# Kernel tuning notes

Hardware: AMD Instinct MI355X
Metric: run time of the kernel (lower is better)

The kernel has to match this reference:

```python
import jax, jax.numpy as jnp
import numpy as np

N_DRUGS = 4096
W_DIM = 512
N_SUB = 10
N_EDGES = 131072


def setup_inputs() -> dict:
    key = jax.random.key(0)
    k1, k2, k3, k4 = jax.random.split(key, 4)
    z_drug = jax.random.normal(k1, (N_DRUGS, W_DIM), dtype=jnp.float32)
    # glorot-ish init for weights
    global_weight = jax.random.normal(k2, (W_DIM, W_DIM), dtype=jnp.float32) * (2.0 / (2 * W_DIM)) ** 0.5
    local_diag = jax.random.normal(k3, (N_SUB, W_DIM), dtype=jnp.float32) * (2.0 / (W_DIM + 1)) ** 0.5
    batch_edges = jax.random.randint(k4, (2, N_EDGES), 0, N_DRUGS, dtype=jnp.int64)
    return {
        "z_drug": z_drug,
        "global_weight": global_weight,
        "local_diag": local_diag,
        "batch_edges": batch_edges,
        "edge_sub_type_idx": 2,
    }


def reference(z_drug, global_weight, local_diag, batch_edges, edge_sub_type_idx):
    # edge_type == 'drug_drug': z1 = z2 = z_drug
    row_embed = z_drug[batch_edges[0]]            # [B, D]
    col_embed = z_drug[batch_edges[1]]            # [B, D]
    d = local_diag[edge_sub_type_idx]             # [D] diagonal of local weight matrix
    # row @ diag(d) @ W @ diag(d) == ((row * d) @ W) * d
    p = ((row_embed * d) @ global_weight) * d     # [B, D]
    # diagonal(p @ col^T) == rowwise dot product
    score = jnp.sum(p * col_embed, axis=-1)       # [B]
    return jax.nn.sigmoid(score)
```

## Files before the change

kernel.cpp:

```cpp
#include <hip/hip_runtime.h>
#include <cstdint>

#define ND 4096
#define D  512

typedef __bf16 bf16x8 __attribute__((ext_vector_type(8)));
typedef float floatx4 __attribute__((ext_vector_type(4)));
typedef unsigned short ushort8 __attribute__((ext_vector_type(8)));

__device__ __forceinline__ float bf2f(unsigned short b) {
    return __uint_as_float(((unsigned int)b) << 16);
}
__device__ __forceinline__ unsigned short f2bf(float f) {
    unsigned int u = __float_as_uint(f);
    u += 0x7fffu + ((u >> 16) & 1u);
    return (unsigned short)(u >> 16);
}
__device__ __forceinline__ float lo16(unsigned int u) { return __uint_as_float(u << 16); }
__device__ __forceinline__ float hi16(unsigned int u) { return __uint_as_float(u & 0xffff0000u); }

__device__ __forceinline__ void gll16(const void* g, void* l) {
    __builtin_amdgcn_global_load_lds((const __attribute__((address_space(1))) unsigned int*)g,
                                     (__attribute__((address_space(3))) unsigned int*)l,
                                     16, 0, 0);
}

union U8B8 { ushort8 u; bf16x8 b; };

__global__ __launch_bounds__(256) void detect_kernel(const unsigned short* __restrict__ z,
                                                     const int* __restrict__ ed,
                                                     int* __restrict__ flags) {
    __shared__ int c0, c1;
    if (threadIdx.x == 0) { c0 = 0; c1 = 0; }
    __syncthreads();
    unsigned short u = z[threadIdx.x];
    int e = (u >> 7) & 0xFF;
    if (e >= 96 && e <= 160) atomicAdd(&c0, 1);
    if (threadIdx.x < 64 && ed[2 * threadIdx.x + 1] == 0) atomicAdd(&c1, 1);
    __syncthreads();
    if (threadIdx.x == 0) {
        flags[0] = (c0 >= 240) ? 1 : 0;
        flags[1] = (c1 >= 56) ? 1 : 0;
    }
}

__global__ __launch_bounds__(256) void make_mt(const void* __restrict__ Wv,
                                               const void* __restrict__ ldv,
                                               const int* __restrict__ sub,
                                               unsigned short* __restrict__ Mt,
                                               const int* __restrict__ flags) {
    __shared__ float lds[64][65];
    int bf = flags[0];
    int su = sub[0];
    if ((unsigned)su > 9u) su = 2;
    int k0 = blockIdx.x * 64, n0 = blockIdx.y * 64;
    int j = threadIdx.x & 63;
    int w = threadIdx.x >> 6;

#pragma unroll
    for (int r = 0; r < 16; r++) {
        int k = k0 + w * 16 + r;
        float v = bf ? bf2f(((const unsigned short*)Wv)[k * D + n0 + j])
                     : ((const float*)Wv)[k * D + n0 + j];
        lds[w * 16 + r][j] = v;
    }
    __syncthreads();

    int k = k0 + j;
    float dk = bf ? bf2f(((const unsigned short*)ldv)[su * D + k])
                  : ((const float*)ldv)[su * D + k];
#pragma unroll
    for (int r = 0; r < 16; r++) {
        int n = n0 + w * 16 + r;
        float dn = bf ? bf2f(((const unsigned short*)ldv)[su * D + n])
                      : ((const float*)ldv)[su * D + n];
        Mt[n * D + k] = f2bf(lds[j][w * 16 + r] * dk * dn);
    }
}

template <bool BF>
__device__ void gemm_body(const void* __restrict__ z,
                          const unsigned short* __restrict__ Mt,
                          unsigned short* __restrict__ Y) {
    __shared__ __bf16 As[64 * 64];
    __shared__ __bf16 Bs[64 * 64];
    int tid = threadIdx.x;
    int w = tid >> 6, lane = tid & 63;
    int rl = lane & 15, quad = lane >> 4;
    int tm = blockIdx.x * 64, tn = blockIdx.y * 64;
    int wm = (w >> 1) * 32, wn = (w & 1) * 32;

    floatx4 acc[2][2] = {};
    for (int kk = 0; kk < D; kk += 64) {
        __syncthreads();
#pragma unroll
        for (int jj = 0; jj < 2; jj++) {
            int rowB = tn + w * 16 + jj * 8 + (lane >> 3);
            int col  = kk + (lane & 7) * 8;
            gll16(Mt + rowB * D + col, &Bs[(w * 16 + jj * 8) * 64]);
            if constexpr (BF) {
                int rowA = tm + w * 16 + jj * 8 + (lane >> 3);
                gll16((const __bf16*)z + rowA * D + col, &As[(w * 16 + jj * 8) * 64]);
            } else {
                int rowA = tm + w * 16 + jj * 8 + (lane >> 3);
                const float* zf = (const float*)z + rowA * D + col;
                float4 f0 = *(const float4*)zf;
                float4 f1 = *(const float4*)(zf + 4);
                U8B8 cv;
                cv.u[0] = f2bf(f0.x); cv.u[1] = f2bf(f0.y); cv.u[2] = f2bf(f0.z); cv.u[3] = f2bf(f0.w);
                cv.u[4] = f2bf(f1.x); cv.u[5] = f2bf(f1.y); cv.u[6] = f2bf(f1.z); cv.u[7] = f2bf(f1.w);
                *(bf16x8*)&As[(w * 16 + jj * 8 + (lane >> 3)) * 64 + (lane & 7) * 8] = cv.b;
            }
        }
        __syncthreads();
#pragma unroll
        for (int kc = 0; kc < 64; kc += 32) {
            bf16x8 a0 = *(const bf16x8*)&As[(wm + rl) * 64 + kc + quad * 8];
            bf16x8 a1 = *(const bf16x8*)&As[(wm + 16 + rl) * 64 + kc + quad * 8];
            bf16x8 b0 = *(const bf16x8*)&Bs[(wn + rl) * 64 + kc + quad * 8];
            bf16x8 b1 = *(const bf16x8*)&Bs[(wn + 16 + rl) * 64 + kc + quad * 8];
            acc[0][0] = __builtin_amdgcn_mfma_f32_16x16x32_bf16(a0, b0, acc[0][0], 0, 0, 0);
            acc[0][1] = __builtin_amdgcn_mfma_f32_16x16x32_bf16(a0, b1, acc[0][1], 0, 0, 0);
            acc[1][0] = __builtin_amdgcn_mfma_f32_16x16x32_bf16(a1, b0, acc[1][0], 0, 0, 0);
            acc[1][1] = __builtin_amdgcn_mfma_f32_16x16x32_bf16(a1, b1, acc[1][1], 0, 0, 0);
        }
    }
#pragma unroll
    for (int j = 0; j < 2; j++) {
        int col = tn + wn + j * 16 + rl;
#pragma unroll
        for (int i = 0; i < 2; i++) {
            int rbase = tm + wm + i * 16 + quad * 4;
#pragma unroll
            for (int r = 0; r < 4; r++)
                Y[(rbase + r) * D + col] = f2bf(acc[i][j][r]);
        }
    }
}

__global__ __launch_bounds__(256) void gemm_kernel(const void* __restrict__ z,
                                                   const unsigned short* __restrict__ Mt,
                                                   unsigned short* __restrict__ Y,
                                                   const int* __restrict__ flags) {
    if (flags[0]) gemm_body<true>(z, Mt, Y);
    else          gemm_body<false>(z, Mt, Y);
}

__global__ __launch_bounds__(256) void edge_pass(const unsigned short* __restrict__ Y,
                                                 const void* __restrict__ z,
                                                 const int* __restrict__ ed,
                                                 float* __restrict__ partial,
                                                 void* __restrict__ out,
                                                 int E,
                                                 const int* __restrict__ flags,
                                                 int pass) {
    int wid = (blockIdx.x * 256 + threadIdx.x) >> 6;
    int lane = threadIdx.x & 63;
    int h = lane >> 5, l = lane & 31;
    int e = wid * 2 + h;
    if (e >= E) return;
    int bf = flags[0];
    int r, c;
    if (flags[1]) { r = ed[2 * e]; c = ed[2 * (E + e)]; }
    else          { r = ed[e];     c = ed[E + e]; }
    r &= ND - 1; c &= ND - 1;

    int col = pass * 256 + l * 8;
    uint4 yu = *(const uint4*)(Y + r * D + col);
    float y0 = lo16(yu.x), y1 = hi16(yu.x), y2 = lo16(yu.y), y3 = hi16(yu.y);
    float y4 = lo16(yu.z), y5 = hi16(yu.z), y6 = lo16(yu.w), y7 = hi16(yu.w);
    float s;
    if (bf) {
        uint4 zu = *(const uint4*)((const unsigned short*)z + c * D + col);
        s  = y0 * lo16(zu.x) + y1 * hi16(zu.x);
        s += y2 * lo16(zu.y) + y3 * hi16(zu.y);
        s += y4 * lo16(zu.z) + y5 * hi16(zu.z);
        s += y6 * lo16(zu.w) + y7 * hi16(zu.w);
    } else {
        const float* zf = (const float*)z + c * D + col;
        float4 f0 = *(const float4*)zf;
        float4 f1 = *(const float4*)(zf + 4);
        s  = y0 * f0.x + y1 * f0.y + y2 * f0.z + y3 * f0.w;
        s += y4 * f1.x + y5 * f1.y + y6 * f1.z + y7 * f1.w;
    }
#pragma unroll
    for (int off = 16; off; off >>= 1)
        s += __shfl_xor(s, off, 64);

    if (l == 0) {
        if (pass == 0) {
            partial[e] = s;
        } else {
            float t = s + partial[e];
            if (!(t > -1e30f && t < 1e30f)) t = 0.0f;
            float sig = 1.0f / (1.0f + __expf(-t));
            if (bf) ((unsigned short*)out)[e] = f2bf(sig);
            else    ((float*)out)[e] = sig;
        }
    }
}

extern "C" void kernel_launch(void* const* d_in, const int* in_sizes, int n_in,
                              void* d_out, int out_size, void* d_ws, size_t ws_size,
                              hipStream_t stream) {
    const void* z     = d_in[0];
    const void* W     = d_in[1];
    const void* ldiag = d_in[2];
    const int* edges  = (const int*)d_in[3];
    const int* sub    = (const int*)d_in[4];
    int E = out_size;

    char* ws = (char*)d_ws;
    unsigned short* Y  = (unsigned short*)ws;
    unsigned short* Mt = (unsigned short*)(ws + 4194304);
    int* flags         = (int*)(ws + 4194304 + 524288);
    float* partial     = (float*)(ws + 4194304 + 524288 + 256);

    detect_kernel<<<1, 256, 0, stream>>>((const unsigned short*)z, edges, flags);
    make_mt<<<dim3(D / 64, D / 64), 256, 0, stream>>>(W, ldiag, sub, Mt, flags);
    gemm_kernel<<<dim3(ND / 64, D / 64), 256, 0, stream>>>(z, Mt, Y, flags);
    int eblocks = (E / 2 + 3) / 4;
    edge_pass<<<eblocks, 256, 0, stream>>>(Y, z, edges, partial, d_out, E, flags, 0);
    edge_pass<<<eblocks, 256, 0, stream>>>(Y, z, edges, partial, d_out, E, flags, 1);
}
```

Before: 122.1 us.

## Inline dtype detection per kernel, re-layout GEMM LDS, split edge pass into four

Drops the separate detection kernel: each kernel now derives the bf16 and int64 flags itself with a wave ballot over the first 64 elements, which removes one launch and the flag round-trip. The GEMM shared-memory tiles switch to a k-block-major layout so each global_load_lds writes 64 rows of one 8-element chunk, changing the LDS read pattern. The edge pass is templated on dtype and index width, uses 16 lanes per edge, and runs in four column slices with partial sums accumulated in memory, so each pass touches a smaller slice of Y and z. This trades one fewer launch for two extra edge launches and extra partial read-modify-write traffic.

Measured after the change: 126.7 us. 3.7% more time.

```diff
diff --git a/kernel.cpp b/kernel.cpp
--- a/kernel.cpp
+++ b/kernel.cpp
@@ -27,30 +27,27 @@
 
 union U8B8 { ushort8 u; bf16x8 b; };
 
-__global__ __launch_bounds__(256) void detect_kernel(const unsigned short* __restrict__ z,
-                                                     const int* __restrict__ ed,
-                                                     int* __restrict__ flags) {
-    __shared__ int c0, c1;
-    if (threadIdx.x == 0) { c0 = 0; c1 = 0; }
-    __syncthreads();
-    unsigned short u = z[threadIdx.x];
+__device__ __forceinline__ int2 detect_flags(const unsigned short* z, const int* ed) {
+    int lane = threadIdx.x & 63;
+    unsigned short u = z[lane];
     int e = (u >> 7) & 0xFF;
-    if (e >= 96 && e <= 160) atomicAdd(&c0, 1);
-    if (threadIdx.x < 64 && ed[2 * threadIdx.x + 1] == 0) atomicAdd(&c1, 1);
-    __syncthreads();
-    if (threadIdx.x == 0) {
-        flags[0] = (c0 >= 240) ? 1 : 0;
-        flags[1] = (c1 >= 56) ? 1 : 0;
-    }
+    unsigned long long b0 = __ballot(e >= 96 && e <= 160);
+    unsigned long long b1 = __ballot(ed[2 * lane + 1] == 0);
+    int2 f;
+    f.x = (__popcll(b0) >= 56) ? 1 : 0;
+    f.y = (__popcll(b1) >= 56) ? 1 : 0;
+    return f;
 }
 
 __global__ __launch_bounds__(256) void make_mt(const void* __restrict__ Wv,
                                                const void* __restrict__ ldv,
                                                const int* __restrict__ sub,
                                                unsigned short* __restrict__ Mt,
-                                               const int* __restrict__ flags) {
+                                               const unsigned short* __restrict__ zdet,
+                                               const int* __restrict__ eddet) {
     __shared__ float lds[64][65];
-    int bf = flags[0];
+    int2 f = detect_flags(zdet, eddet);
+    int bf = f.x;
     int su = sub[0];
     if ((unsigned)su > 9u) su = 2;
     int k0 = blockIdx.x * 64, n0 = blockIdx.y * 64;
@@ -82,8 +79,8 @@
 __device__ void gemm_body(const void* __restrict__ z,
                           const unsigned short* __restrict__ Mt,
                           unsigned short* __restrict__ Y) {
-    __shared__ __bf16 As[64 * 64];
-    __shared__ __bf16 Bs[64 * 64];
+    __shared__ __bf16 As[8 * 512];
+    __shared__ __bf16 Bs[8 * 512];
     int tid = threadIdx.x;
     int w = tid >> 6, lane = tid & 63;
     int rl = lane & 15, quad = lane >> 4;
@@ -94,31 +91,29 @@
     for (int kk = 0; kk < D; kk += 64) {
         __syncthreads();
 #pragma unroll
-        for (int jj = 0; jj < 2; jj++) {
-            int rowB = tn + w * 16 + jj * 8 + (lane >> 3);
-            int col  = kk + (lane & 7) * 8;
-            gll16(Mt + rowB * D + col, &Bs[(w * 16 + jj * 8) * 64]);
+        for (int t = 0; t < 2; t++) {
+            int kb = w * 2 + t;
+            gll16(Mt + (tn + lane) * D + kk + kb * 8, Bs + kb * 512);
             if constexpr (BF) {
-                int rowA = tm + w * 16 + jj * 8 + (lane >> 3);
-                gll16((const __bf16*)z + rowA * D + col, &As[(w * 16 + jj * 8) * 64]);
+                gll16((const __bf16*)z + (tm + lane) * D + kk + kb * 8, As + kb * 512);
             } else {
-                int rowA = tm + w * 16 + jj * 8 + (lane >> 3);
-                const float* zf = (const float*)z + rowA * D + col;
+                const float* zf = (const float*)z + (tm + lane) * D + kk + kb * 8;
                 float4 f0 = *(const float4*)zf;
                 float4 f1 = *(const float4*)(zf + 4);
                 U8B8 cv;
                 cv.u[0] = f2bf(f0.x); cv.u[1] = f2bf(f0.y); cv.u[2] = f2bf(f0.z); cv.u[3] = f2bf(f0.w);
                 cv.u[4] = f2bf(f1.x); cv.u[5] = f2bf(f1.y); cv.u[6] = f2bf(f1.z); cv.u[7] = f2bf(f1.w);
-                *(bf16x8*)&As[(w * 16 + jj * 8 + (lane >> 3)) * 64 + (lane & 7) * 8] = cv.b;
+                *(bf16x8*)(As + kb * 512 + lane * 8) = cv.b;
             }
         }
         __syncthreads();
 #pragma unroll
         for (int kc = 0; kc < 64; kc += 32) {
-            bf16x8 a0 = *(const bf16x8*)&As[(wm + rl) * 64 + kc + quad * 8];
-            bf16x8 a1 = *(const bf16x8*)&As[(wm + 16 + rl) * 64 + kc + quad * 8];
-            bf16x8 b0 = *(const bf16x8*)&Bs[(wn + rl) * 64 + kc + quad * 8];
-            bf16x8 b1 = *(const bf16x8*)&Bs[(wn + 16 + rl) * 64 + kc + quad * 8];
+            int kb0 = kc >> 3;
+            bf16x8 a0 = *(const bf16x8*)(As + (kb0 + quad) * 512 + (wm + rl) * 8);
+            bf16x8 a1 = *(const bf16x8*)(As + (kb0 + quad) * 512 + (wm + 16 + rl) * 8);
+            bf16x8 b0 = *(const bf16x8*)(Bs + (kb0 + quad) * 512 + (wn + rl) * 8);
+            bf16x8 b1 = *(const bf16x8*)(Bs + (kb0 + quad) * 512 + (wn + 16 + rl) * 8);
             acc[0][0] = __builtin_amdgcn_mfma_f32_16x16x32_bf16(a0, b0, acc[0][0], 0, 0, 0);
             acc[0][1] = __builtin_amdgcn_mfma_f32_16x16x32_bf16(a0, b1, acc[0][1], 0, 0, 0);
             acc[1][0] = __builtin_amdgcn_mfma_f32_16x16x32_bf16(a1, b0, acc[1][0], 0, 0, 0);
@@ -141,36 +136,35 @@
 __global__ __launch_bounds__(256) void gemm_kernel(const void* __restrict__ z,
                                                    const unsigned short* __restrict__ Mt,
                                                    unsigned short* __restrict__ Y,
-                                                   const int* __restrict__ flags) {
-    if (flags[0]) gemm_body<true>(z, Mt, Y);
-    else          gemm_body<false>(z, Mt, Y);
-}
-
-__global__ __launch_bounds__(256) void edge_pass(const unsigned short* __restrict__ Y,
-                                                 const void* __restrict__ z,
-                                                 const int* __restrict__ ed,
-                                                 float* __restrict__ partial,
-                                                 void* __restrict__ out,
-                                                 int E,
-                                                 const int* __restrict__ flags,
-                                                 int pass) {
-    int wid = (blockIdx.x * 256 + threadIdx.x) >> 6;
+                                                   const int* __restrict__ eddet) {
+    int2 f = detect_flags((const unsigned short*)z, eddet);
+    if (f.x) gemm_body<true>(z, Mt, Y);
+    else     gemm_body<false>(z, Mt, Y);
+}
+
+template <bool BF, bool I64>
+__device__ void edge_body(const unsigned short* __restrict__ Y,
+                          const void* __restrict__ z,
+                          const int* __restrict__ ed,
+                          float* __restrict__ partial,
+                          void* __restrict__ out,
+                          int E, int pass) {
+    int gid = blockIdx.x * 256 + threadIdx.x;
     int lane = threadIdx.x & 63;
-    int h = lane >> 5, l = lane & 31;
-    int e = wid * 2 + h;
+    int e = (gid >> 6) * 4 + (lane >> 4);
+    int l = lane & 15;
     if (e >= E) return;
-    int bf = flags[0];
     int r, c;
-    if (flags[1]) { r = ed[2 * e]; c = ed[2 * (E + e)]; }
-    else          { r = ed[e];     c = ed[E + e]; }
+    if constexpr (I64) { r = ed[2 * e]; c = ed[2 * (E + e)]; }
+    else               { r = ed[e];     c = ed[E + e]; }
     r &= ND - 1; c &= ND - 1;
 
-    int col = pass * 256 + l * 8;
+    int col = pass * 128 + l * 8;
     uint4 yu = *(const uint4*)(Y + r * D + col);
     float y0 = lo16(yu.x), y1 = hi16(yu.x), y2 = lo16(yu.y), y3 = hi16(yu.y);
     float y4 = lo16(yu.z), y5 = hi16(yu.z), y6 = lo16(yu.w), y7 = hi16(yu.w);
     float s;
-    if (bf) {
+    if constexpr (BF) {
         uint4 zu = *(const uint4*)((const unsigned short*)z + c * D + col);
         s  = y0 * lo16(zu.x) + y1 * hi16(zu.x);
         s += y2 * lo16(zu.y) + y3 * hi16(zu.y);
@@ -184,20 +178,33 @@
         s += y4 * f1.x + y5 * f1.y + y6 * f1.z + y7 * f1.w;
     }
 #pragma unroll
-    for (int off = 16; off; off >>= 1)
+    for (int off = 8; off; off >>= 1)
         s += __shfl_xor(s, off, 64);
 
     if (l == 0) {
-        if (pass == 0) {
-            partial[e] = s;
-        } else {
+        if (pass == 0)      partial[e] = s;
+        else if (pass < 3)  partial[e] += s;
+        else {
             float t = s + partial[e];
             if (!(t > -1e30f && t < 1e30f)) t = 0.0f;
             float sig = 1.0f / (1.0f + __expf(-t));
-            if (bf) ((unsigned short*)out)[e] = f2bf(sig);
-            else    ((float*)out)[e] = sig;
-        }
-    }
+            if constexpr (BF) ((unsigned short*)out)[e] = f2bf(sig);
+            else              ((float*)out)[e] = sig;
+        }
+    }
+}
+
+__global__ __launch_bounds__(256) void edge_kernel(const unsigned short* __restrict__ Y,
+                                                   const void* __restrict__ z,
+                                                   const int* __restrict__ ed,
+                                                   float* __restrict__ partial,
+                                                   void* __restrict__ out,
+                                                   int E, int pass) {
+    int2 f = detect_flags((const unsigned short*)z, ed);
+    if (f.x) { if (f.y) edge_body<true, true>(Y, z, ed, partial, out, E, pass);
+               else     edge_body<true, false>(Y, z, ed, partial, out, E, pass); }
+    else     { if (f.y) edge_body<false, true>(Y, z, ed, partial, out, E, pass);
+               else     edge_body<false, false>(Y, z, ed, partial, out, E, pass); }
 }
 
 extern "C" void kernel_launch(void* const* d_in, const int* in_sizes, int n_in,
@@ -213,13 +220,12 @@
     char* ws = (char*)d_ws;
     unsigned short* Y  = (unsigned short*)ws;
     unsigned short* Mt = (unsigned short*)(ws + 4194304);
-    int* flags         = (int*)(ws + 4194304 + 524288);
-    float* partial     = (float*)(ws + 4194304 + 524288 + 256);
-
-    detect_kernel<<<1, 256, 0, stream>>>((const unsigned short*)z, edges, flags);
-    make_mt<<<dim3(D / 64, D / 64), 256, 0, stream>>>(W, ldiag, sub, Mt, flags);
-    gemm_kernel<<<dim3(ND / 64, D / 64), 256, 0, stream>>>(z, Mt, Y, flags);
-    int eblocks = (E / 2 + 3) / 4;
-    edge_pass<<<eblocks, 256, 0, stream>>>(Y, z, edges, partial, d_out, E, flags, 0);
-    edge_pass<<<eblocks, 256, 0, stream>>>(Y, z, edges, partial, d_out, E, flags, 1);
-}
+    float* partial     = (float*)(ws + 4194304 + 524288);
+
+    make_mt<<<dim3(D / 64, D / 64), 256, 0, stream>>>(W, ldiag, sub, Mt,
+                                                      (const unsigned short*)z, edges);
+    gemm_kernel<<<dim3(ND / 64, D / 64), 256, 0, stream>>>(z, Mt, Y, edges);
+    int eblocks = (E + 15) / 16;
+    for (int p = 0; p < 4; p++)
+        edge_kernel<<<eblocks, 256, 0, stream>>>(Y, z, edges, partial, d_out, E, p);
+}
```
